# Optimization experiments

Hardware: AMD Instinct MI355X
Metric: run time of the kernel (lower is better)

The kernel has to match this reference:

```python
import jax, jax.numpy as jnp
import numpy as np

B, S, D, H, DK = 2, 2048, 2048, 16, 128
ALIBI_SLOPE = 8.0
NEG = -1e9  # finite stand-in for -inf so gradients stay finite


def setup_inputs() -> dict:
    key = jax.random.key(0)
    ks = jax.random.split(key, 8)
    states = jax.random.normal(ks[0], (B, S, D), jnp.float32)
    # causal ALiBi-style additive bias: -(i-j) for j<=i else very negative
    pos = jnp.arange(S)
    dist = pos[None, :] - pos[:, None]  # j - i
    bias = jnp.where(dist <= 0, dist.astype(jnp.float32), NEG)
    bias_mask = jnp.broadcast_to(bias[None], (B, S, S))
    # per-head scale: exp2(-((h+1)*slope/H))
    head_scale = jnp.exp2(-((jnp.arange(H) + 1.0) * ALIBI_SLOPE / H)).astype(jnp.float32)
    init = lambda k, shp: jax.random.normal(k, shp, jnp.float32) * (shp[-1] ** -0.5)
    return {
        'states': states,
        'bias_mask': bias_mask,
        'head_scale': head_scale,
        'Wq': init(ks[1], (D, D)), 'bq': jnp.zeros((D,), jnp.float32),
        'Wk': init(ks[2], (D, D)), 'bk': jnp.zeros((D,), jnp.float32),
        'Wv': init(ks[3], (D, D)), 'bv': jnp.zeros((D,), jnp.float32),
        'Wg': init(ks[4], (H, D)), 'bg': jnp.zeros((H,), jnp.float32),
        'Wo': init(ks[5], (D, D)), 'bo': jnp.zeros((D,), jnp.float32),
    }


def reference(states, bias_mask, head_scale, Wq, bq, Wk, bk, Wv, bv, Wg, bg, Wo, bo):
    b, s, d = states.shape
    key_scale = DK ** -0.5
    proj = lambda x, W, bias: x @ W.T + bias
    # [b,s,d] -> [b,h,s,dk]
    q = proj(states, Wq, bq).reshape(b, s, H, DK).transpose(0, 2, 1, 3)
    k = proj(states, Wk, bk).reshape(b, s, H, DK).transpose(0, 2, 1, 3)
    v = proj(states, Wv, bv).reshape(b, s, H, DK).transpose(0, 2, 1, 3)
    # additive per-head ALiBi bias: [b,1,s,s] * [1,h,1,1]
    bias = bias_mask[:, None, :, :] * head_scale[None, :, None, None]
    scores = jnp.einsum('bhqd,bhkd->bhqk', q, k) * key_scale + bias
    attn = jax.nn.softmax(scores, axis=-1)
    o = jnp.einsum('bhqk,bhkd->bhqd', attn, v).transpose(0, 2, 1, 3)  # [b,s,h,dk]
    g = jax.nn.sigmoid(proj(states, Wg, bg))  # [b,s,h]
    o = o * g[..., None]
    return proj(o.reshape(b, s, d), Wo, bo)
```

## Files before the change

### kernel.cpp

```cpp
#include <hip/hip_runtime.h>

#define SEQ  2048
#define NROW 4096
#define KDIM 2048
#define NH   16
#define DKH  128
#define CSUB 20.0f
#define LOG2E 1.44269504088896f

typedef unsigned int u32;
typedef unsigned short u16;
typedef __attribute__((ext_vector_type(8))) __bf16 bf16x8;
typedef __attribute__((ext_vector_type(4))) float f32x4;
typedef __attribute__((ext_vector_type(4))) u16 u16x4;

struct alignas(16) U4 { u32 x, y, z, w; };

__device__ __forceinline__ u16 f2bf(float f) {
  u32 u = __builtin_bit_cast(u32, f);
  u32 r = (u + 0x7fffu + ((u >> 16) & 1u)) >> 16;
  return (u16)r;
}
__device__ __forceinline__ u16 f2bf_n(float f) {
  __bf16 h = (__bf16)f;
  return __builtin_bit_cast(u16, h);
}
__device__ __forceinline__ bf16x8 asb(U4 v) { return __builtin_bit_cast(bf16x8, v); }
__device__ __forceinline__ float exp2a(float x) {
  float r;
  asm("v_exp_f32 %0, %1" : "=v"(r) : "v"(x));
  return r;
}

__device__ __forceinline__ void gl2lds16(const u16* g, u16* l) {
  __builtin_amdgcn_global_load_lds(
      (const __attribute__((address_space(1))) void*)g,
      (__attribute__((address_space(3))) void*)l, 16, 0, 0);
}

__global__ __launch_bounds__(256)
void cvtk(const float* __restrict__ src, u16* __restrict__ dst, int n)
{
  const int i = (blockIdx.x * 256 + threadIdx.x) * 4;
  if (i < n) {
    f32x4 v = *(const f32x4*)(src + i);
    u16x4 o;
#pragma unroll
    for (int j = 0; j < 4; ++j) o[j] = f2bf(v[j]);
    *(u16x4*)(dst + i) = o;
  }
}

__global__ __launch_bounds__(256, 2)
void qkvg(const u16* __restrict__ A, const u16* __restrict__ B,
          const float* __restrict__ bq, const float* __restrict__ bk,
          const float* __restrict__ bv, u16* __restrict__ Qw,
          u16* __restrict__ Kw, u16* __restrict__ Vw)
{
  __shared__ alignas(16) u16 As[128 * 32];
  __shared__ alignas(16) u16 Bs[128 * 32];
  const int tid = threadIdx.x;
  const int lane = tid & 63, wave = tid >> 6;
  const int wm = wave >> 1, wn = wave & 1;
  const int l15 = lane & 15, quad = lane >> 4;
  const int m0 = blockIdx.y * 128, n0 = blockIdx.x * 128;

  f32x4 acc[4][4];
#pragma unroll
  for (int i = 0; i < 4; ++i)
#pragma unroll
    for (int j = 0; j < 4; ++j) acc[i][j] = {0.f, 0.f, 0.f, 0.f};

  const int gr = lane >> 2;
  const int gc = (lane & 3) * 8;

  for (int kk = 0; kk < KDIM; kk += 32) {
#pragma unroll
    for (int it = 0; it < 2; ++it) {
      const int r0 = wave * 32 + it * 16;
      gl2lds16(A + (size_t)(m0 + r0 + gr) * KDIM + kk + gc, As + r0 * 32);
      gl2lds16(B + (size_t)(n0 + r0 + gr) * KDIM + kk + gc, Bs + r0 * 32);
    }
    __syncthreads();
    U4 af[4], bg[4];
#pragma unroll
    for (int t = 0; t < 4; ++t) {
      af[t] = *(const U4*)(As + (wm * 64 + t * 16 + l15) * 32 + quad * 8);
      bg[t] = *(const U4*)(Bs + (wn * 64 + t * 16 + l15) * 32 + quad * 8);
    }
#pragma unroll
    for (int mt = 0; mt < 4; ++mt)
#pragma unroll
      for (int nt = 0; nt < 4; ++nt)
        acc[mt][nt] = __builtin_amdgcn_mfma_f32_16x16x32_bf16(
            asb(af[mt]), asb(bg[nt]), acc[mt][nt], 0, 0, 0);
    __syncthreads();
  }

  const int seg = n0 >> 11;
  const float* bp = seg == 0 ? bq : (seg == 1 ? bk : bv);
  u16* Cq = seg == 0 ? Qw : Kw;

#pragma unroll
  for (int mt = 0; mt < 4; ++mt) {
    const int rowb = m0 + wm * 64 + mt * 16 + quad * 4;
    const int b = rowb >> 11, srow = rowb & (SEQ - 1);
#pragma unroll
    for (int nt = 0; nt < 4; ++nt) {
      const int col6 = n0 + wn * 64 + nt * 16 + l15;
      const int col = col6 & 2047;
      const int h = col >> 7, dk = col & 127;
      const float bvl = bp[col];
      if (seg == 2) {
        u16x4 pk;
#pragma unroll
        for (int r = 0; r < 4; ++r) pk[r] = f2bf(acc[mt][nt][r] + bvl);
        const size_t idx = ((size_t)(b * NH + h) * DKH + dk) * SEQ + srow;
        *(u16x4*)(Vw + idx) = pk;
      } else {
#pragma unroll
        for (int r = 0; r < 4; ++r) {
          const size_t idx = ((size_t)(b * NH + h) * SEQ + (srow + r)) * DKH + dk;
          Cq[idx] = f2bf(acc[mt][nt][r] + bvl);
        }
      }
    }
  }
}

__global__ __launch_bounds__(256, 2)
void gemm_bt(const u16* __restrict__ A, const u16* __restrict__ B,
             const float* __restrict__ bias, float* __restrict__ Cf)
{
  __shared__ alignas(16) u16 As[128 * 32];
  __shared__ alignas(16) u16 Bs[128 * 32];
  const int tid = threadIdx.x;
  const int lane = tid & 63, wave = tid >> 6;
  const int wm = wave >> 1, wn = wave & 1;
  const int l15 = lane & 15, quad = lane >> 4;
  const int m0 = blockIdx.y * 128, n0 = blockIdx.x * 128;

  f32x4 acc[4][4];
#pragma unroll
  for (int i = 0; i < 4; ++i)
#pragma unroll
    for (int j = 0; j < 4; ++j) acc[i][j] = {0.f, 0.f, 0.f, 0.f};

  const int gr = lane >> 2;
  const int gc = (lane & 3) * 8;

  for (int kk = 0; kk < KDIM; kk += 32) {
#pragma unroll
    for (int it = 0; it < 2; ++it) {
      const int r0 = wave * 32 + it * 16;
      gl2lds16(A + (size_t)(m0 + r0 + gr) * KDIM + kk + gc, As + r0 * 32);
      gl2lds16(B + (size_t)(n0 + r0 + gr) * KDIM + kk + gc, Bs + r0 * 32);
    }
    __syncthreads();
    U4 af[4], bg[4];
#pragma unroll
    for (int t = 0; t < 4; ++t) {
      af[t] = *(const U4*)(As + (wm * 64 + t * 16 + l15) * 32 + quad * 8);
      bg[t] = *(const U4*)(Bs + (wn * 64 + t * 16 + l15) * 32 + quad * 8);
    }
#pragma unroll
    for (int mt = 0; mt < 4; ++mt)
#pragma unroll
      for (int nt = 0; nt < 4; ++nt)
        acc[mt][nt] = __builtin_amdgcn_mfma_f32_16x16x32_bf16(
            asb(af[mt]), asb(bg[nt]), acc[mt][nt], 0, 0, 0);
    __syncthreads();
  }

#pragma unroll
  for (int mt = 0; mt < 4; ++mt) {
    const int rowb = m0 + wm * 64 + mt * 16 + quad * 4;
#pragma unroll
    for (int nt = 0; nt < 4; ++nt) {
      const int col = n0 + wn * 64 + nt * 16 + l15;
      const float bv = bias[col];
#pragma unroll
      for (int r = 0; r < 4; ++r)
        Cf[(size_t)(rowb + r) * KDIM + col] = acc[mt][nt][r] + bv;
    }
  }
}

__global__ __launch_bounds__(256)
void gateg(const u16* __restrict__ X, const float* __restrict__ Wg,
           const float* __restrict__ bg, float* __restrict__ G)
{
  __shared__ float red[4][16][16];
  const int tid = threadIdx.x;
  const int lane = tid & 63, wave = tid >> 6;
  const int l15 = lane & 15, quad = lane >> 4;
  const int m0 = blockIdx.x * 16;

  const u16*  Xp = X + (size_t)(m0 + l15) * KDIM + wave * 512 + quad * 8;
  const float* Wp = Wg + (size_t)l15 * KDIM + wave * 512 + quad * 8;

  f32x4 acc = {0.f, 0.f, 0.f, 0.f};
#pragma unroll
  for (int kk = 0; kk < 512; kk += 32) {
    U4 a = *(const U4*)(Xp + kk);
    f32x4 w0 = *(const f32x4*)(Wp + kk);
    f32x4 w1 = *(const f32x4*)(Wp + kk + 4);
    U4 bw;
    bw.x = (u32)f2bf(w0[0]) | ((u32)f2bf(w0[1]) << 16);
    bw.y = (u32)f2bf(w0[2]) | ((u32)f2bf(w0[3]) << 16);
    bw.z = (u32)f2bf(w1[0]) | ((u32)f2bf(w1[1]) << 16);
    bw.w = (u32)f2bf(w1[2]) | ((u32)f2bf(w1[3]) << 16);
    acc = __builtin_amdgcn_mfma_f32_16x16x32_bf16(asb(a), asb(bw), acc, 0, 0, 0);
  }
#pragma unroll
  for (int r = 0; r < 4; ++r) red[wave][quad * 4 + r][l15] = acc[r];
  __syncthreads();
  const int row = tid >> 4, head = tid & 15;
  float s = bg[head];
#pragma unroll
  for (int w = 0; w < 4; ++w) s += red[w][row][head];
  G[(size_t)(m0 + row) * NH + head] = 1.f / (1.f + __expf(-s));
}

__device__ __forceinline__ void stage_kv(const u16* __restrict__ Kh,
                                         const u16* __restrict__ Vh,
                                         int kk, u16* Ksb, u16* Vsb,
                                         int wave, int lane)
{
  const int rK = lane >> 4, cK = lane & 15;
  const int rV = lane >> 3, cV = lane & 7;
#pragma unroll
  for (int j = 0; j < 4; ++j) {
    const int r0k = wave * 16 + j * 4;
    const int xk = ((j & 1) << 2) | rK;
    gl2lds16(Kh + (size_t)(kk + r0k + rK) * DKH + ((cK ^ xk) * 8),
             Ksb + r0k * 128);
    const int r0v = wave * 32 + j * 8;
    gl2lds16(Vh + (size_t)(r0v + rV) * SEQ + kk + ((cV ^ rV) * 8),
             Vsb + r0v * 64);
  }
}

__global__ __launch_bounds__(256, 2)
void attnk(const u16* __restrict__ Q, const u16* __restrict__ Km,
           const u16* __restrict__ Vt, const float* __restrict__ hsc,
           const float* __restrict__ G, u16* __restrict__ O)
{
  __shared__ alignas(16) u16 Ks[2][64 * 128];
  __shared__ alignas(16) u16 Vs[2][128 * 64];
  __shared__ alignas(16) u16 Ps[4][16 * 72];
  const int tid = threadIdx.x;
  const int lane = tid & 63, wave = tid >> 6;
  const int l15 = lane & 15, quad = lane >> 4;
  const int l7x = l15 & 7;
  const int qt = 31 - blockIdx.y, bh = blockIdx.x;
  const int b = bh >> 4, h = bh & 15;
  const size_t hoff = (size_t)bh * SEQ * DKH;
  const u16* Qh = Q + hoff;
  const u16* Kh = Km + hoff;
  const u16* Vh = Vt + hoff;
  const float hs2 = hsc[h] * LOG2E;
  const float ks2 = 0.08838834764831845f * LOG2E;
  const float csub2 = CSUB * LOG2E;
  const float dstep = 64.0f * hs2;

  const int q0 = qt * 64 + wave * 16;
  const int ntile = qt + 1;

  U4 aq[4];
#pragma unroll
  for (int c = 0; c < 4; ++c)
    aq[c] = *(const U4*)(Qh + (size_t)(q0 + l15) * DKH + c * 32 + quad * 8);

  float base[4][4];
#pragma unroll
  for (int r = 0; r < 4; ++r) {
    const int i = q0 + quad * 4 + r;
#pragma unroll
    for (int nt = 0; nt < 4; ++nt)
      base[r][nt] = (float)(nt * 16 + l15 - i) * hs2 - csub2;
  }

  f32x4 oacc[8];
#pragma unroll
  for (int c = 0; c < 8; ++c) oacc[c] = {0.f, 0.f, 0.f, 0.f};
  float l_lane[4] = {0.f, 0.f, 0.f, 0.f};

  stage_kv(Kh, Vh, 0, Ks[0], Vs[0], wave, lane);

  for (int t = 0; t < ntile; ++t) {
    const int kk = t * 64;
    const int cb = t & 1;
    __syncthreads();
    if (t + 1 < ntile)
      stage_kv(Kh, Vh, kk + 64, Ks[cb ^ 1], Vs[cb ^ 1], wave, lane);

    f32x4 sf[4];
#pragma unroll
    for (int nt = 0; nt < 4; ++nt) {
      f32x4 s = {0.f, 0.f, 0.f, 0.f};
#pragma unroll
      for (int c = 0; c < 4; ++c) {
        U4 bk = *(const U4*)(Ks[cb] + (nt * 16 + l15) * 128 +
                             (((c * 4 + quad) ^ l7x) * 8));
        s = __builtin_amdgcn_mfma_f32_16x16x32_bf16(asb(aq[c]), asb(bk), s, 0, 0, 0);
      }
      sf[nt] = s;
    }

    u16* Pw = &Ps[wave][0];
    const float tf = (float)t;
    if (t + 1 < ntile) {
#pragma unroll
      for (int r = 0; r < 4; ++r) {
#pragma unroll
        for (int nt = 0; nt < 4; ++nt) {
          const float p = exp2a(fmaf(sf[nt][r], ks2, fmaf(tf, dstep, base[r][nt])));
          l_lane[r] += p;
          Pw[(quad * 4 + r) * 72 + nt * 16 + l15] = f2bf_n(p);
        }
      }
    } else {
#pragma unroll
      for (int r = 0; r < 4; ++r) {
        const int i = q0 + quad * 4 + r;
#pragma unroll
        for (int nt = 0; nt < 4; ++nt) {
          const int j = kk + nt * 16 + l15;
          float p = 0.f;
          if (j <= i)
            p = exp2a(fmaf(sf[nt][r], ks2, fmaf(tf, dstep, base[r][nt])));
          l_lane[r] += p;
          Pw[(quad * 4 + r) * 72 + nt * 16 + l15] = f2bf_n(p);
        }
      }
    }
    asm volatile("s_waitcnt lgkmcnt(0)" ::: "memory");
    __builtin_amdgcn_sched_barrier(0);
    U4 pf0 = *(const U4*)(Pw + l15 * 72 + quad * 8);
    U4 pf1 = *(const U4*)(Pw + l15 * 72 + 32 + quad * 8);
#pragma unroll
    for (int c = 0; c < 8; ++c) {
      U4 bv0 = *(const U4*)(Vs[cb] + (c * 16 + l15) * 64 + ((quad ^ l7x) * 8));
      U4 bv1 = *(const U4*)(Vs[cb] + (c * 16 + l15) * 64 + (((quad + 4) ^ l7x) * 8));
      oacc[c] = __builtin_amdgcn_mfma_f32_16x16x32_bf16(asb(pf0), asb(bv0), oacc[c], 0, 0, 0);
      oacc[c] = __builtin_amdgcn_mfma_f32_16x16x32_bf16(asb(pf1), asb(bv1), oacc[c], 0, 0, 0);
    }
  }

  float sc[4];
#pragma unroll
  for (int r = 0; r < 4; ++r) {
#pragma unroll
    for (int d = 1; d < 16; d <<= 1)
      l_lane[r] += __shfl_xor(l_lane[r], d, 64);
    const int i = q0 + quad * 4 + r;
    sc[r] = G[(size_t)(b * SEQ + i) * NH + h] / l_lane[r];
  }

  __syncthreads();
  u16* OL = &Ks[0][0] + wave * 2112;
#pragma unroll
  for (int c = 0; c < 8; ++c)
#pragma unroll
    for (int r = 0; r < 4; ++r)
      OL[(quad * 4 + r) * 132 + c * 16 + l15] = f2bf_n(oacc[c][r] * sc[r]);
  __syncthreads();
#pragma unroll
  for (int o = 0; o < 4; ++o) {
    const int row = o * 4 + quad;
    U4 val = *(const U4*)(OL + row * 132 + l15 * 8);
    *(U4*)(O + ((size_t)(b * SEQ + q0 + row) * NH + h) * DKH + l15 * 8) = val;
  }
}

extern "C" void kernel_launch(void* const* d_in, const int* in_sizes, int n_in,
                              void* d_out, int out_size, void* d_ws, size_t ws_size,
                              hipStream_t stream)
{
  const float* states = (const float*)d_in[0];
  const float* hscale = (const float*)d_in[2];
  const float* Wq = (const float*)d_in[3];
  const float* bq = (const float*)d_in[4];
  const float* Wk = (const float*)d_in[5];
  const float* bk = (const float*)d_in[6];
  const float* Wv = (const float*)d_in[7];
  const float* bv = (const float*)d_in[8];
  const float* Wg = (const float*)d_in[9];
  const float* bg = (const float*)d_in[10];
  const float* Wo = (const float*)d_in[11];
  const float* bo = (const float*)d_in[12];
  float* out = (float*)d_out;

  char* ws = (char*)d_ws;
  const size_t MB = 1024 * 1024;
  u16* S16  = (u16*)(ws);
  u16* Qw   = (u16*)(ws + 16 * MB);
  u16* Kw   = (u16*)(ws + 32 * MB);
  u16* Vw   = (u16*)(ws + 48 * MB);
  u16* W16  = (u16*)(ws + 64 * MB);
  u16* Ow   = (u16*)(ws + 64 * MB);
  u16* Wo16 = (u16*)(ws + 80 * MB);
  float* Gw = out;

  const int NW = KDIM * KDIM;
  const int NS = NROW * KDIM;
  dim3 blk(256);

  cvtk<<<dim3(NS / 1024), blk, 0, stream>>>(states, S16, NS);
  gateg<<<dim3(NROW / 16), blk, 0, stream>>>(S16, Wg, bg, Gw);
  cvtk<<<dim3(NW / 1024), blk, 0, stream>>>(Wq, W16, NW);
  cvtk<<<dim3(NW / 1024), blk, 0, stream>>>(Wk, W16 + NW, NW);
  cvtk<<<dim3(NW / 1024), blk, 0, stream>>>(Wv, W16 + 2 * (size_t)NW, NW);
  qkvg<<<dim3(48, 32), blk, 0, stream>>>(S16, W16, bq, bk, bv, Qw, Kw, Vw);
  attnk<<<dim3(32, 32), blk, 0, stream>>>(Qw, Kw, Vw, hscale, Gw, Ow);
  cvtk<<<dim3(NW / 1024), blk, 0, stream>>>(Wo, Wo16, NW);
  gemm_bt<<<dim3(16, 32), blk, 0, stream>>>(Ow, Wo16, bo, out);
}
```

Measured before the change: 420.9 us.

## Fuse states conversion into gate kernel, batch weight casts, add MFMA priority hints

```diff
diff --git a/kernel.cpp b/kernel.cpp
--- a/kernel.cpp
+++ b/kernel.cpp
@@ -46,9 +46,78 @@
     f32x4 v = *(const f32x4*)(src + i);
     u16x4 o;
 #pragma unroll
-    for (int j = 0; j < 4; ++j) o[j] = f2bf(v[j]);
+    for (int j = 0; j < 4; ++j) o[j] = f2bf_n(v[j]);
     *(u16x4*)(dst + i) = o;
   }
+}
+
+__global__ __launch_bounds__(256)
+void cvt3k(const float* __restrict__ s0, const float* __restrict__ s1,
+           const float* __restrict__ s2, u16* __restrict__ dst, int n)
+{
+  const float* s = blockIdx.y == 0 ? s0 : (blockIdx.y == 1 ? s1 : s2);
+  u16* d = dst + (size_t)blockIdx.y * n;
+  const int i = (blockIdx.x * 256 + threadIdx.x) * 4;
+  if (i < n) {
+    f32x4 v = *(const f32x4*)(s + i);
+    u16x4 o;
+#pragma unroll
+    for (int j = 0; j < 4; ++j) o[j] = f2bf_n(v[j]);
+    *(u16x4*)(d + i) = o;
+  }
+}
+
+__global__ __launch_bounds__(256)
+void gatesg(const float* __restrict__ X, const float* __restrict__ Wg,
+            const float* __restrict__ bg, float* __restrict__ G,
+            u16* __restrict__ S16)
+{
+  __shared__ alignas(16) u16 xs16[16 * 2056];
+  __shared__ float red[4][16][16];
+  const int tid = threadIdx.x;
+  const int lane = tid & 63, wave = tid >> 6;
+  const int l15 = lane & 15, quad = lane >> 4;
+  const int m0 = blockIdx.x * 16;
+
+#pragma unroll
+  for (int r = 0; r < 16; ++r) {
+    const size_t gofs = (size_t)(m0 + r) * KDIM + tid * 8;
+    f32x4 v0 = *(const f32x4*)(X + gofs);
+    f32x4 v1 = *(const f32x4*)(X + gofs + 4);
+    U4 o;
+    o.x = (u32)f2bf_n(v0[0]) | ((u32)f2bf_n(v0[1]) << 16);
+    o.y = (u32)f2bf_n(v0[2]) | ((u32)f2bf_n(v0[3]) << 16);
+    o.z = (u32)f2bf_n(v1[0]) | ((u32)f2bf_n(v1[1]) << 16);
+    o.w = (u32)f2bf_n(v1[2]) | ((u32)f2bf_n(v1[3]) << 16);
+    *(U4*)(S16 + gofs) = o;
+    *(U4*)(&xs16[r * 2056 + tid * 8]) = o;
+  }
+  __syncthreads();
+
+  const u16*   Xp = &xs16[l15 * 2056 + wave * 512 + quad * 8];
+  const float* Wp = Wg + (size_t)l15 * KDIM + wave * 512 + quad * 8;
+
+  f32x4 acc = {0.f, 0.f, 0.f, 0.f};
+#pragma unroll
+  for (int kk = 0; kk < 512; kk += 32) {
+    U4 a = *(const U4*)(Xp + kk);
+    f32x4 w0 = *(const f32x4*)(Wp + kk);
+    f32x4 w1 = *(const f32x4*)(Wp + kk + 4);
+    U4 bw;
+    bw.x = (u32)f2bf_n(w0[0]) | ((u32)f2bf_n(w0[1]) << 16);
+    bw.y = (u32)f2bf_n(w0[2]) | ((u32)f2bf_n(w0[3]) << 16);
+    bw.z = (u32)f2bf_n(w1[0]) | ((u32)f2bf_n(w1[1]) << 16);
+    bw.w = (u32)f2bf_n(w1[2]) | ((u32)f2bf_n(w1[3]) << 16);
+    acc = __builtin_amdgcn_mfma_f32_16x16x32_bf16(asb(a), asb(bw), acc, 0, 0, 0);
+  }
+#pragma unroll
+  for (int r = 0; r < 4; ++r) red[wave][quad * 4 + r][l15] = acc[r];
+  __syncthreads();
+  const int row = tid >> 4, head = tid & 15;
+  float s = bg[head];
+#pragma unroll
+  for (int w = 0; w < 4; ++w) s += red[w][row][head];
+  G[(size_t)(m0 + row) * NH + head] = 1.f / (1.f + __expf(-s));
 }
 
 __global__ __launch_bounds__(256, 2)
@@ -82,18 +151,18 @@
       gl2lds16(B + (size_t)(n0 + r0 + gr) * KDIM + kk + gc, Bs + r0 * 32);
     }
     __syncthreads();
-    U4 af[4], bg[4];
+    U4 af[4], bg4[4];
 #pragma unroll
     for (int t = 0; t < 4; ++t) {
-      af[t] = *(const U4*)(As + (wm * 64 + t * 16 + l15) * 32 + quad * 8);
-      bg[t] = *(const U4*)(Bs + (wn * 64 + t * 16 + l15) * 32 + quad * 8);
+      af[t]  = *(const U4*)(As + (wm * 64 + t * 16 + l15) * 32 + quad * 8);
+      bg4[t] = *(const U4*)(Bs + (wn * 64 + t * 16 + l15) * 32 + quad * 8);
     }
 #pragma unroll
     for (int mt = 0; mt < 4; ++mt)
 #pragma unroll
       for (int nt = 0; nt < 4; ++nt)
         acc[mt][nt] = __builtin_amdgcn_mfma_f32_16x16x32_bf16(
-            asb(af[mt]), asb(bg[nt]), acc[mt][nt], 0, 0, 0);
+            asb(af[mt]), asb(bg4[nt]), acc[mt][nt], 0, 0, 0);
     __syncthreads();
   }
 
@@ -114,14 +183,14 @@
       if (seg == 2) {
         u16x4 pk;
 #pragma unroll
-        for (int r = 0; r < 4; ++r) pk[r] = f2bf(acc[mt][nt][r] + bvl);
+        for (int r = 0; r < 4; ++r) pk[r] = f2bf_n(acc[mt][nt][r] + bvl);
         const size_t idx = ((size_t)(b * NH + h) * DKH + dk) * SEQ + srow;
         *(u16x4*)(Vw + idx) = pk;
       } else {
 #pragma unroll
         for (int r = 0; r < 4; ++r) {
           const size_t idx = ((size_t)(b * NH + h) * SEQ + (srow + r)) * DKH + dk;
-          Cq[idx] = f2bf(acc[mt][nt][r] + bvl);
+          Cq[idx] = f2bf_n(acc[mt][nt][r] + bvl);
         }
       }
     }
@@ -157,18 +226,18 @@
       gl2lds16(B + (size_t)(n0 + r0 + gr) * KDIM + kk + gc, Bs + r0 * 32);
     }
     __syncthreads();
-    U4 af[4], bg[4];
+    U4 af[4], bg4[4];
 #pragma unroll
     for (int t = 0; t < 4; ++t) {
-      af[t] = *(const U4*)(As + (wm * 64 + t * 16 + l15) * 32 + quad * 8);
-      bg[t] = *(const U4*)(Bs + (wn * 64 + t * 16 + l15) * 32 + quad * 8);
+      af[t]  = *(const U4*)(As + (wm * 64 + t * 16 + l15) * 32 + quad * 8);
+      bg4[t] = *(const U4*)(Bs + (wn * 64 + t * 16 + l15) * 32 + quad * 8);
     }
 #pragma unroll
     for (int mt = 0; mt < 4; ++mt)
 #pragma unroll
       for (int nt = 0; nt < 4; ++nt)
         acc[mt][nt] = __builtin_amdgcn_mfma_f32_16x16x32_bf16(
-            asb(af[mt]), asb(bg[nt]), acc[mt][nt], 0, 0, 0);
+            asb(af[mt]), asb(bg4[nt]), acc[mt][nt], 0, 0, 0);
     __syncthreads();
   }
 
@@ -184,42 +253,6 @@
         Cf[(size_t)(rowb + r) * KDIM + col] = acc[mt][nt][r] + bv;
     }
   }
-}
-
-__global__ __launch_bounds__(256)
-void gateg(const u16* __restrict__ X, const float* __restrict__ Wg,
-           const float* __restrict__ bg, float* __restrict__ G)
-{
-  __shared__ float red[4][16][16];
-  const int tid = threadIdx.x;
-  const int lane = tid & 63, wave = tid >> 6;
-  const int l15 = lane & 15, quad = lane >> 4;
-  const int m0 = blockIdx.x * 16;
-
-  const u16*  Xp = X + (size_t)(m0 + l15) * KDIM + wave * 512 + quad * 8;
-  const float* Wp = Wg + (size_t)l15 * KDIM + wave * 512 + quad * 8;
-
-  f32x4 acc = {0.f, 0.f, 0.f, 0.f};
-#pragma unroll
-  for (int kk = 0; kk < 512; kk += 32) {
-    U4 a = *(const U4*)(Xp + kk);
-    f32x4 w0 = *(const f32x4*)(Wp + kk);
-    f32x4 w1 = *(const f32x4*)(Wp + kk + 4);
-    U4 bw;
-    bw.x = (u32)f2bf(w0[0]) | ((u32)f2bf(w0[1]) << 16);
-    bw.y = (u32)f2bf(w0[2]) | ((u32)f2bf(w0[3]) << 16);
-    bw.z = (u32)f2bf(w1[0]) | ((u32)f2bf(w1[1]) << 16);
-    bw.w = (u32)f2bf(w1[2]) | ((u32)f2bf(w1[3]) << 16);
-    acc = __builtin_amdgcn_mfma_f32_16x16x32_bf16(asb(a), asb(bw), acc, 0, 0, 0);
-  }
-#pragma unroll
-  for (int r = 0; r < 4; ++r) red[wave][quad * 4 + r][l15] = acc[r];
-  __syncthreads();
-  const int row = tid >> 4, head = tid & 15;
-  float s = bg[head];
-#pragma unroll
-  for (int w = 0; w < 4; ++w) s += red[w][row][head];
-  G[(size_t)(m0 + row) * NH + head] = 1.f / (1.f + __expf(-s));
 }
 
 __device__ __forceinline__ void stage_kv(const u16* __restrict__ Kh,
@@ -296,6 +329,7 @@
       stage_kv(Kh, Vh, kk + 64, Ks[cb ^ 1], Vs[cb ^ 1], wave, lane);
 
     f32x4 sf[4];
+    __builtin_amdgcn_s_setprio(1);
 #pragma unroll
     for (int nt = 0; nt < 4; ++nt) {
       f32x4 s = {0.f, 0.f, 0.f, 0.f};
@@ -307,6 +341,7 @@
       }
       sf[nt] = s;
     }
+    __builtin_amdgcn_s_setprio(0);
 
     u16* Pw = &Ps[wave][0];
     const float tf = (float)t;
@@ -339,6 +374,7 @@
     __builtin_amdgcn_sched_barrier(0);
     U4 pf0 = *(const U4*)(Pw + l15 * 72 + quad * 8);
     U4 pf1 = *(const U4*)(Pw + l15 * 72 + 32 + quad * 8);
+    __builtin_amdgcn_s_setprio(1);
 #pragma unroll
     for (int c = 0; c < 8; ++c) {
       U4 bv0 = *(const U4*)(Vs[cb] + (c * 16 + l15) * 64 + ((quad ^ l7x) * 8));
@@ -346,6 +382,7 @@
       oacc[c] = __builtin_amdgcn_mfma_f32_16x16x32_bf16(asb(pf0), asb(bv0), oacc[c], 0, 0, 0);
       oacc[c] = __builtin_amdgcn_mfma_f32_16x16x32_bf16(asb(pf1), asb(bv1), oacc[c], 0, 0, 0);
     }
+    __builtin_amdgcn_s_setprio(0);
   }
 
   float sc[4];
@@ -400,20 +437,16 @@
   u16* Vw   = (u16*)(ws + 48 * MB);
   u16* W16  = (u16*)(ws + 64 * MB);
   u16* Ow   = (u16*)(ws + 64 * MB);
-  u16* Wo16 = (u16*)(ws + 80 * MB);
+  u16* Wo16 = (u16*)(ws);
   float* Gw = out;
 
   const int NW = KDIM * KDIM;
-  const int NS = NROW * KDIM;
   dim3 blk(256);
 
-  cvtk<<<dim3(NS / 1024), blk, 0, stream>>>(states, S16, NS);
-  gateg<<<dim3(NROW / 16), blk, 0, stream>>>(S16, Wg, bg, Gw);
-  cvtk<<<dim3(NW / 1024), blk, 0, stream>>>(Wq, W16, NW);
-  cvtk<<<dim3(NW / 1024), blk, 0, stream>>>(Wk, W16 + NW, NW);
-  cvtk<<<dim3(NW / 1024), blk, 0, stream>>>(Wv, W16 + 2 * (size_t)NW, NW);
+  gatesg<<<dim3(NROW / 16), blk, 0, stream>>>(states, Wg, bg, Gw, S16);
+  cvt3k<<<dim3(NW / 1024, 3), blk, 0, stream>>>(Wq, Wk, Wv, W16, NW);
   qkvg<<<dim3(48, 32), blk, 0, stream>>>(S16, W16, bq, bk, bv, Qw, Kw, Vw);
+  cvtk<<<dim3(NW / 1024), blk, 0, stream>>>(Wo, Wo16, NW);
   attnk<<<dim3(32, 32), blk, 0, stream>>>(Qw, Kw, Vw, hscale, Gw, Ow);
-  cvtk<<<dim3(NW / 1024), blk, 0, stream>>>(Wo, Wo16, NW);
   gemm_bt<<<dim3(16, 32), blk, 0, stream>>>(Ow, Wo16, bo, out);
 }
```

Result: no change. 413.9 us (-1.6%).
